# Kernel tuning notes

Hardware: AMD Instinct MI355X
Metric: run time of the kernel (lower is better)

## Reference

```python
import jax, jax.numpy as jnp
import numpy as np

B, E, D, L, R = 32, 30000, 200, 50, 474
GAMMA, ALPHA, BETA = 9.0, 0.3, 0.7


def _gate(x_ent, x_lit, Wg, bg, W1, W2, gate_bias):
    # Gate module: x = [x_ent; x_lit]; out = (1-g)*x_ent + g*tanh(Linear(x))
    x = jnp.concatenate([x_ent, x_lit], axis=-1)
    g_emb = jnp.tanh(x @ Wg.T + bg)
    g = jax.nn.sigmoid(x_ent @ W1.T + x_lit @ W2.T + gate_bias)
    return (1.0 - g) * x_ent + g * g_emb


def setup_inputs() -> dict:
    key = jax.random.key(0)
    ks = jax.random.split(key, 11)
    rn = lambda k, shape: jax.random.normal(k, shape, jnp.float32) * 0.05
    return {
        'e1': jax.random.randint(ks[0], (B,), 0, E),
        'rel': jax.random.randint(ks[1], (B,), 0, R),
        'e2_multi': jax.random.randint(ks[2], (B, E), 0, 2).astype(jnp.int32),
        'emb_e': rn(ks[3], (E, D)),
        'emb_rel': rn(ks[4], (R, D)),
        'num_lit': jax.random.uniform(ks[5], (E, L), jnp.float32),
        'Wg': rn(ks[6], (D, D + L)),
        'bg': jnp.zeros((D,), jnp.float32),
        'W1': rn(ks[7], (D, D)),
        'W2': rn(ks[8], (D, L)),
        'gate_bias': jnp.zeros((D,), jnp.float32),
        'prob': jax.random.uniform(ks[9], (B, E), jnp.float32),
        'drop_mask': jax.random.randint(ks[10], (B, E), 0, 2).astype(jnp.float32),
    }


def reference(e1, rel, e2_multi, emb_e, emb_rel, num_lit, Wg, bg, W1, W2,
              gate_bias, prob, drop_mask):
    e2m = e2_multi.astype(emb_e.dtype)  # [B, E] multi-hot labels
    # literal-gated embeddings (inp_drop treated as eval/identity)
    e1_emb = _gate(emb_e[e1], num_lit[e1], Wg, bg, W1, W2, gate_bias)   # [B, D]
    e2_emb = _gate(emb_e, num_lit, Wg, bg, W1, W2, gate_bias)           # [E, D]
    rel_emb = emb_rel[rel]                                              # [B, D]

    # our_loss: weighted masked means over the full entity table
    e2p = e2m * prob                                                    # [B, E]
    pos_mean = (e2p @ e2_emb) / e2p.sum(-1, keepdims=True)              # [B, D]
    pos_mean = ALPHA * pos_mean + (1.0 - ALPHA) * e1_emb
    inv = 1.0 - e2m
    inv_drop = inv * drop_mask * 2.0  # F.dropout(p=0.5) = mask * 1/(1-p)
    neg_mean = (inv_drop @ e2_emb) / inv.sum(-1, keepdims=True)
    neg_mean = BETA * neg_mean + (1.0 - BETA) * e1_emb

    q = e1_emb + rel_emb                                                # [B, D]
    pos_s = jnp.abs(q - pos_mean).sum(-1, keepdims=True)                # [B, 1]
    neg_s = jnp.abs(q - neg_mean).sum(-1)                               # [B]
    # faithful to torch: [B] - [B,1] broadcasts to [B,B]
    loss = -jnp.mean(jax.nn.log_sigmoid(neg_s - pos_s))

    # broadcast L1 distance to ALL entities: [B, E, D] intermediate
    score = GAMMA - jnp.abs(q[:, None, :] - e2_emb[None, :, :]).sum(-1)  # [B, E]
    pred = jax.nn.sigmoid(score)
    return (pred, loss)
```

## Files before the change

### kernel.cpp

```cpp
#include <hip/hip_runtime.h>
#include <hip/hip_bf16.h>
#include <cstddef>

constexpr int B = 32, E = 30000, D = 200, L = 50;

using short8 = __attribute__((ext_vector_type(8))) short;
using f32x4  = __attribute__((ext_vector_type(4))) float;

__device__ __forceinline__ float sigmoidf_(float x){ return 1.f/(1.f+__expf(-x)); }
__device__ __forceinline__ float tanhf_(float x){
    float t = __expf(-2.f*fabsf(x));
    return copysignf((1.f-t)/(1.f+t), x);
}
__device__ __forceinline__ unsigned short f2bf(float x){
    unsigned u = __float_as_uint(x);
    u += 0x7fffu + ((u>>16)&1u);
    return (unsigned short)(u>>16);
}
__device__ __forceinline__ float bf2f(unsigned short h){
    return __uint_as_float(((unsigned)h)<<16);
}

constexpr int WELEMS = 26*8*64*8;

__global__ __launch_bounds__(256) void wprep_kernel(
    const float* __restrict__ Wg, const float* __restrict__ W1,
    const float* __restrict__ W2,
    unsigned short* __restrict__ whi, unsigned short* __restrict__ wlo)
{
    int idx = blockIdx.x*256 + threadIdx.x;
    if (idx >= WELEMS) return;
    int j = idx & 7, l = (idx>>3)&63, ks = (idx>>9)&7, nt = idx>>12;
    int n = nt*16 + (l&15);
    int k = ks*32 + ((l>>4)&3)*8 + j;
    float v = 0.f;
    if (n < 208) {
        int d = n;
        if (d < 200 && k < 250) v = Wg[d*250 + k];
    } else {
        int d = n - 208;
        if (d < 200) {
            if (k < 200)      v = W1[d*200 + k];
            else if (k < 250) v = W2[d*50 + (k-200)];
        }
    }
    unsigned short h = f2bf(v);
    whi[idx] = h;
    wlo[idx] = f2bf(v - bf2f(h));
}

__global__ __launch_bounds__(256) void sums_kernel(
    const int* __restrict__ e2m, const float* __restrict__ prob,
    float* __restrict__ psum8, float* __restrict__ isum8)
{
    const int tid = threadIdx.x;
    const int b = blockIdx.x >> 3, ch = blockIdx.x & 7;
    const int es = ch * 3750;
    const int*   mrow = e2m  + (size_t)b * E + es;
    const float* prow = prob + (size_t)b * E + es;
    float sp = 0.f, si = 0.f;
    for (int i = tid; i < 3750; i += 256) {
        float m = (float)mrow[i];
        sp = fmaf(m, prow[i], sp);
        si += (1.f - m);
    }
    #pragma unroll
    for (int off = 32; off >= 1; off >>= 1) {
        sp += __shfl_down(sp, off);
        si += __shfl_down(si, off);
    }
    __shared__ float rp[4], ri[4];
    if ((tid & 63) == 0) { rp[tid >> 6] = sp; ri[tid >> 6] = si; }
    __syncthreads();
    if (tid == 0) {
        psum8[b*8 + ch] = rp[0] + rp[1] + rp[2] + rp[3];
        isum8[b*8 + ch] = ri[0] + ri[1] + ri[2] + ri[3];
    }
}

__global__ __launch_bounds__(512) void gate_kernel(
    const float* __restrict__ emb_e, const float* __restrict__ num_lit,
    const unsigned short* __restrict__ whi, const unsigned short* __restrict__ wlo,
    const float* __restrict__ bg, const float* __restrict__ gbias,
    float* __restrict__ e2_emb)
{
    __shared__ __align__(16) char smem[28672];
    unsigned short* Ah = (unsigned short*)smem;
    unsigned short* Al = (unsigned short*)(smem + 8192);
    float* PW = (float*)smem;

    const int tid  = threadIdx.x;
    const int lane = tid & 63;
    const int wid  = tid >> 6;
    const int mt   = wid & 3;
    const int g    = wid >> 2;
    const int mb   = blockIdx.x >> 1;
    const int h    = blockIdx.x & 1;
    const int e0   = mb * 64;
    const int start = h * 6;
    const int ntb  = start + g * 13;

    f32x4 acc[7];
    #pragma unroll
    for (int i = 0; i < 7; ++i) acc[i] = (f32x4){0.f,0.f,0.f,0.f};

    const int srow = tid >> 3;
    const int skq  = tid & 7;
    const int se   = e0 + srow;
    const int aoff = (((srow >> 4)*2 + (skq >> 2))*64 + ((srow & 15) | ((skq & 3) << 4)))*8;

#define WOFF(p, ks) (((size_t)(((ntb + (p))*8 + c*2 + (ks))*64 + lane))*8)

    for (int c = 0; c < 4; ++c) {
        float v[8];
        const int k0 = c*64 + skq*8;
        if (se < E) {
            if (k0 + 7 < 200) {
                float4 f0 = *(const float4*)(emb_e + (size_t)se*200 + k0);
                float4 f1 = *(const float4*)(emb_e + (size_t)se*200 + k0 + 4);
                v[0]=f0.x; v[1]=f0.y; v[2]=f0.z; v[3]=f0.w;
                v[4]=f1.x; v[5]=f1.y; v[6]=f1.z; v[7]=f1.w;
            } else {
                #pragma unroll
                for (int z = 0; z < 8; ++z) {
                    int kz = k0 + z;
                    v[z] = (kz < 250) ? num_lit[(size_t)se*50 + (kz - 200)] : 0.f;
                }
            }
        } else {
            #pragma unroll
            for (int z = 0; z < 8; ++z) v[z] = 0.f;
        }
        if (c) __syncthreads();
        short8 hv, lv;
        #pragma unroll
        for (int z = 0; z < 8; ++z) {
            unsigned short hh = f2bf(v[z]);
            hv[z] = (short)hh;
            lv[z] = (short)f2bf(v[z] - bf2f(hh));
        }
        *(short8*)&Ah[aoff] = hv;
        *(short8*)&Al[aoff] = lv;
        __syncthreads();

        short8 pwh[2][2], pwl[2][2];
        pwh[0][0] = *(const short8*)(whi + WOFF(0,0));
        pwh[0][1] = *(const short8*)(whi + WOFF(0,1));
        pwl[0][0] = *(const short8*)(wlo + WOFF(0,0));
        pwl[0][1] = *(const short8*)(wlo + WOFF(0,1));

        short8 xh[2], xl[2];
        #pragma unroll
        for (int ks = 0; ks < 2; ++ks) {
            int fo = ((mt*2 + ks)*64 + lane)*8;
            xh[ks] = *(const short8*)&Ah[fo];
            xl[ks] = *(const short8*)&Al[fo];
        }

        #pragma unroll
        for (int p = 0; p < 7; ++p) {
            const int cur = p & 1, nxt = cur ^ 1;
            if (p < 6) {
                pwh[nxt][0] = *(const short8*)(whi + WOFF(p+1,0));
                pwh[nxt][1] = *(const short8*)(whi + WOFF(p+1,1));
                pwl[nxt][0] = *(const short8*)(wlo + WOFF(p+1,0));
                pwl[nxt][1] = *(const short8*)(wlo + WOFF(p+1,1));
            }
            #pragma unroll
            for (int ks = 0; ks < 2; ++ks) {
                acc[p] = __builtin_amdgcn_mfma_f32_16x16x32_bf16(xh[ks], pwh[cur][ks], acc[p], 0,0,0);
                acc[p] = __builtin_amdgcn_mfma_f32_16x16x32_bf16(xl[ks], pwh[cur][ks], acc[p], 0,0,0);
                acc[p] = __builtin_amdgcn_mfma_f32_16x16x32_bf16(xh[ks], pwl[cur][ks], acc[p], 0,0,0);
            }
        }
    }
#undef WOFF

    __syncthreads();
    if (g == 1) {
        #pragma unroll
        for (int p = 0; p < 7; ++p)
            *(f32x4*)&PW[((mt*7 + p)*64 + lane)*4] = acc[p];
    }
    __syncthreads();
    if (g == 0) {
        const int col = lane & 15, rg = lane >> 4;
        #pragma unroll
        for (int p = 0; p < 7; ++p) {
            int d = (start + p)*16 + col;
            if (d >= 200) continue;
            float bgd = bg[d], gbd = gbias[d];
            f32x4 p2 = *(const f32x4*)&PW[((mt*7 + p)*64 + lane)*4];
            #pragma unroll
            for (int r = 0; r < 4; ++r) {
                int e = e0 + mt*16 + rg*4 + r;
                if (e >= E) continue;
                float pre1 = acc[p][r] + bgd;
                float pre2 = p2[r] + gbd;
                float gt = sigmoidf_(pre2);
                float t  = tanhf_(pre1);
                float emb = emb_e[(size_t)e*200 + d];
                e2_emb[(size_t)e*200 + d] = (1.f - gt)*emb + gt*t;
            }
        }
    }
}

__global__ __launch_bounds__(256) void q_kernel(
    const int* __restrict__ e1, const int* __restrict__ rel,
    const float* __restrict__ emb_rel, const float* __restrict__ e2_emb,
    float* __restrict__ q)
{
    int tid = threadIdx.x;
    for (int idx = tid; idx < B * D; idx += 256) {
        int b = idx / D, d = idx % D;
        q[idx] = e2_emb[(size_t)e1[b] * D + d] + emb_rel[(size_t)rel[b] * D + d];
    }
}

constexpr int GVB = 235;

__global__ __launch_bounds__(256) void gemv_kernel(
    const int* __restrict__ e2m, const float* __restrict__ prob,
    const float* __restrict__ drop, const float* __restrict__ e2_emb,
    float* __restrict__ gpart)
{
    __shared__ unsigned short Bf[13312];
    __shared__ unsigned short Acp[2048], Acn[2048];
    const int tid = threadIdx.x, lane = tid & 63, w = tid >> 6;
    const int e0 = blockIdx.x * 128;

    f32x4 acc[2][2][4];
    #pragma unroll
    for (int a = 0; a < 2; ++a)
        #pragma unroll
        for (int m = 0; m < 2; ++m)
            #pragma unroll
            for (int s = 0; s < 4; ++s) acc[a][m][s] = (f32x4){0.f,0.f,0.f,0.f};

    for (int c = 0; c < 2; ++c) {
        const int ec = e0 + c*64;
        if (c) __syncthreads();

        {
            const int bb = tid >> 3, part = tid & 7;
            const int eb = ec + part*8;
            float cp[8], cn[8];
            size_t base = (size_t)bb * E + eb;
            if (eb + 7 < E) {
                int4   m0 = *(const int4*)(e2m + base),   m1 = *(const int4*)(e2m + base + 4);
                float4 p0 = *(const float4*)(prob + base), p1 = *(const float4*)(prob + base + 4);
                float4 d0 = *(const float4*)(drop + base), d1 = *(const float4*)(drop + base + 4);
                cp[0]=m0.x?p0.x:0.f; cn[0]=m0.x?0.f:2.f*d0.x;
                cp[1]=m0.y?p0.y:0.f; cn[1]=m0.y?0.f:2.f*d0.y;
                cp[2]=m0.z?p0.z:0.f; cn[2]=m0.z?0.f:2.f*d0.z;
                cp[3]=m0.w?p0.w:0.f; cn[3]=m0.w?0.f:2.f*d0.w;
                cp[4]=m1.x?p1.x:0.f; cn[4]=m1.x?0.f:2.f*d1.x;
                cp[5]=m1.y?p1.y:0.f; cn[5]=m1.y?0.f:2.f*d1.y;
                cp[6]=m1.z?p1.z:0.f; cn[6]=m1.z?0.f:2.f*d1.z;
                cp[7]=m1.w?p1.w:0.f; cn[7]=m1.w?0.f:2.f*d1.w;
            } else {
                #pragma unroll
                for (int j = 0; j < 8; ++j) {
                    int e = eb + j;
                    cp[j] = 0.f; cn[j] = 0.f;
                    if (e < E) {
                        int m = e2m[base + j];
                        cp[j] = m ? prob[base + j] : 0.f;
                        cn[j] = m ? 0.f : 2.f * drop[base + j];
                    }
                }
            }
            short8 scp, scn;
            #pragma unroll
            for (int j = 0; j < 8; ++j) { scp[j] = (short)f2bf(cp[j]); scn[j] = (short)f2bf(cn[j]); }
            int off = (((bb >> 4)*2 + (part >> 2))*64 + ((bb & 15) | ((part & 3) << 4)))*8;
            *(short8*)&Acp[off] = scp;
            *(short8*)&Acn[off] = scn;
        }

        for (int s = tid; s < 3328; s += 256) {
            int el = s / 52, d4 = (s - el*52)*4;
            int e = ec + el;
            float4 f = make_float4(0.f,0.f,0.f,0.f);
            if (e < E && d4 < 200) f = *(const float4*)(e2_emb + (size_t)e*200 + d4);
            int ks = el >> 5, lp = (el >> 3) & 3, j = el & 7;
            float fv[4] = {f.x, f.y, f.z, f.w};
            #pragma unroll
            for (int z = 0; z < 4; ++z) {
                int d = d4 + z;
                Bf[(((d >> 4)*2 + ks)*64 + ((d & 15) | (lp << 4)))*8 + j] = f2bf(fv[z]);
            }
        }
        __syncthreads();

        short8 cpA[2][2], cnA[2][2];
        #pragma unroll
        for (int mtb = 0; mtb < 2; ++mtb)
            #pragma unroll
            for (int ks = 0; ks < 2; ++ks) {
                int fo = ((mtb*2 + ks)*64 + lane)*8;
                cpA[mtb][ks] = *(const short8*)&Acp[fo];
                cnA[mtb][ks] = *(const short8*)&Acn[fo];
            }
        #pragma unroll
        for (int ks = 0; ks < 2; ++ks)
            #pragma unroll
            for (int slot = 0; slot < 4; ++slot) {
                int nt = w + slot*4;
                if (nt < 13) {
                    short8 bf = *(const short8*)&Bf[((nt*2 + ks)*64 + lane)*8];
                    acc[0][0][slot] = __builtin_amdgcn_mfma_f32_16x16x32_bf16(cpA[0][ks], bf, acc[0][0][slot], 0,0,0);
                    acc[0][1][slot] = __builtin_amdgcn_mfma_f32_16x16x32_bf16(cpA[1][ks], bf, acc[0][1][slot], 0,0,0);
                    acc[1][0][slot] = __builtin_amdgcn_mfma_f32_16x16x32_bf16(cnA[0][ks], bf, acc[1][0][slot], 0,0,0);
                    acc[1][1][slot] = __builtin_amdgcn_mfma_f32_16x16x32_bf16(cnA[1][ks], bf, acc[1][1][slot], 0,0,0);
                }
            }
    }

    const int col = lane & 15, rg = lane >> 4;
    #pragma unroll
    for (int mat = 0; mat < 2; ++mat)
        #pragma unroll
        for (int mtb = 0; mtb < 2; ++mtb)
            #pragma unroll
            for (int slot = 0; slot < 4; ++slot) {
                int nt = w + slot*4;
                if (nt >= 13) continue;
                int d = nt*16 + col;
                if (d >= 200) continue;
                #pragma unroll
                for (int r = 0; r < 4; ++r) {
                    int b = mtb*16 + rg*4 + r;
                    gpart[(((size_t)blockIdx.x*2 + mat)*32 + b)*200 + d]
                        = acc[mat][mtb][slot][r];
                }
            }
}

__global__ __launch_bounds__(128) void gred_kernel(
    const float* __restrict__ gpart, float* __restrict__ posv, float* __restrict__ negv)
{
    int o = blockIdx.x*128 + threadIdx.x;
    float sp = 0.f, sn = 0.f;
    #pragma unroll 4
    for (int blk = 0; blk < GVB; ++blk) {
        sp += gpart[((size_t)blk*2 + 0)*6400 + o];
        sn += gpart[((size_t)blk*2 + 1)*6400 + o];
    }
    posv[o] = sp;
    negv[o] = sn;
}

__global__ __launch_bounds__(256) void score_kernel(
    const float* __restrict__ q, const float* __restrict__ e2_emb,
    float* __restrict__ pred)
{
    __shared__ __align__(16) float Qs[32*204];
    const int tid = threadIdx.x;
    const int e0 = blockIdx.x * 64;
    for (int i = tid; i < B*D; i += 256) {
        int b = i / 200, d = i - b*200;
        Qs[b*204 + d] = q[i];
    }
    __syncthreads();

    const int bgrp = tid & 7, egrp = tid >> 3;
    const int b0 = bgrp*4;
    const int ea = e0 + egrp*2, eb = ea + 1;
    const float* r0 = e2_emb + (size_t)(ea < E ? ea : E-1)*200;
    const float* r1 = e2_emb + (size_t)(eb < E ? eb : E-1)*200;

    float acc0[4] = {0.f,0.f,0.f,0.f}, acc1[4] = {0.f,0.f,0.f,0.f};
    #pragma unroll 5
    for (int dc = 0; dc < 200; dc += 8) {
        float4 a0 = *(const float4*)(r0 + dc);
        float4 a1 = *(const float4*)(r0 + dc + 4);
        float4 b0v = *(const float4*)(r1 + dc);
        float4 b1v = *(const float4*)(r1 + dc + 4);
        #pragma unroll
        for (int i = 0; i < 4; ++i) {
            float4 qa = *(const float4*)&Qs[(b0+i)*204 + dc];
            float4 qb = *(const float4*)&Qs[(b0+i)*204 + dc + 4];
            acc0[i] += fabsf(qa.x-a0.x) + fabsf(qa.y-a0.y) + fabsf(qa.z-a0.z) + fabsf(qa.w-a0.w)
                     + fabsf(qb.x-a1.x) + fabsf(qb.y-a1.y) + fabsf(qb.z-a1.z) + fabsf(qb.w-a1.w);
            acc1[i] += fabsf(qa.x-b0v.x) + fabsf(qa.y-b0v.y) + fabsf(qa.z-b0v.z) + fabsf(qa.w-b0v.w)
                     + fabsf(qb.x-b1v.x) + fabsf(qb.y-b1v.y) + fabsf(qb.z-b1v.z) + fabsf(qb.w-b1v.w);
        }
    }
    #pragma unroll
    for (int i = 0; i < 4; ++i) {
        if (ea < E) pred[(size_t)(b0+i)*E + ea] = sigmoidf_(9.0f - acc0[i]);
        if (eb < E) pred[(size_t)(b0+i)*E + eb] = sigmoidf_(9.0f - acc1[i]);
    }
}

__global__ __launch_bounds__(256) void final_kernel(
    const int* __restrict__ e1, const float* __restrict__ q,
    const float* __restrict__ posv, const float* __restrict__ negv,
    const float* __restrict__ psum8, const float* __restrict__ isum8,
    const float* __restrict__ e2_emb, float* __restrict__ loss_out)
{
    const int tid = threadIdx.x;
    __shared__ float SP[32], SI[32];
    if (tid < 32) {
        float s = 0.f, t = 0.f;
        #pragma unroll
        for (int k = 0; k < 8; ++k) { s += psum8[tid*8 + k]; t += isum8[tid*8 + k]; }
        SP[tid] = s; SI[tid] = t;
    }
    __syncthreads();

    const int b = tid >> 3, dl = tid & 7;
    const int e1b = e1[b];
    const float isp = 1.f / SP[b];
    const float isn = 1.f / SI[b];
    float ps = 0.f, ns = 0.f;
    #pragma unroll
    for (int t = 0; t < 25; ++t) {
        int d = dl*25 + t;
        float e1e = e2_emb[(size_t)e1b*200 + d];
        float pm = 0.3f * (posv[b*200 + d] * isp) + 0.7f * e1e;
        float nm = 0.7f * (negv[b*200 + d] * isn) + 0.3f * e1e;
        float qv = q[b*200 + d];
        ps += fabsf(qv - pm);
        ns += fabsf(qv - nm);
    }
    ps += __shfl_down(ps, 4, 8); ps += __shfl_down(ps, 2, 8); ps += __shfl_down(ps, 1, 8);
    ns += __shfl_down(ns, 4, 8); ns += __shfl_down(ns, 2, 8); ns += __shfl_down(ns, 1, 8);

    __shared__ float PS[B], NS[B];
    if (dl == 0) { PS[b] = ps; NS[b] = ns; }
    __syncthreads();

    float part = 0.f;
    #pragma unroll
    for (int r = 0; r < 4; ++r) {
        int idx = tid + r*256;
        int i = idx >> 5, j = idx & 31;
        float x = NS[j] - PS[i];
        part += fminf(x, 0.f) - log1pf(expf(-fabsf(x)));
    }
    #pragma unroll
    for (int off = 32; off >= 1; off >>= 1) part += __shfl_down(part, off);
    __shared__ float wr[4];
    if ((tid & 63) == 0) wr[tid >> 6] = part;
    __syncthreads();
    if (tid == 0) loss_out[0] = -(wr[0] + wr[1] + wr[2] + wr[3]) * (1.f/1024.f);
}

extern "C" void kernel_launch(void* const* d_in, const int* in_sizes, int n_in,
                              void* d_out, int out_size, void* d_ws, size_t ws_size,
                              hipStream_t stream)
{
    const int*   e1      = (const int*)d_in[0];
    const int*   rel     = (const int*)d_in[1];
    const int*   e2m     = (const int*)d_in[2];
    const float* emb_e   = (const float*)d_in[3];
    const float* emb_rel = (const float*)d_in[4];
    const float* num_lit = (const float*)d_in[5];
    const float* Wg      = (const float*)d_in[6];
    const float* bg      = (const float*)d_in[7];
    const float* W1      = (const float*)d_in[8];
    const float* W2      = (const float*)d_in[9];
    const float* gbias   = (const float*)d_in[10];
    const float* prob    = (const float*)d_in[11];
    const float* drop    = (const float*)d_in[12];

    float* pred = (float*)d_out;
    float* ws   = (float*)d_ws;

    float*          e2_emb = ws;
    float*          q      = ws + 6000000;
    unsigned short* whi    = (unsigned short*)(ws + 6006400);
    unsigned short* wlo    = (unsigned short*)(ws + 6059648);
    float*          gpart  = ws + 6112896;
    float*          posv   = ws + 9120896;
    float*          negv   = ws + 9127296;
    float*          psum8  = ws + 9133696;
    float*          isum8  = ws + 9133952;

    wprep_kernel<<<WELEMS/256, 256, 0, stream>>>(Wg, W1, W2, whi, wlo);
    sums_kernel<<<256, 256, 0, stream>>>(e2m, prob, psum8, isum8);
    gate_kernel<<<944, 512, 0, stream>>>(emb_e, num_lit, whi, wlo, bg, gbias, e2_emb);
    q_kernel<<<1, 256, 0, stream>>>(e1, rel, emb_rel, e2_emb, q);
    gemv_kernel<<<GVB, 256, 0, stream>>>(e2m, prob, drop, e2_emb, gpart);
    gred_kernel<<<50, 128, 0, stream>>>(gpart, posv, negv);
    score_kernel<<<(E + 63)/64, 256, 0, stream>>>(q, e2_emb, pred);
    final_kernel<<<1, 256, 0, stream>>>(e1, q, posv, negv, psum8, isum8, e2_emb,
                                        pred + (size_t)B*E);
}
```

Measured before the change: 268.3 us.

## Load gate A-fragments directly to registers and restage score kernel over entities

The gate kernel now loads each lane's MFMA A-fragment straight from global memory and splits it into bf16 hi/lo with a truncation-based perm split, dropping the LDS staging and per-chunk barriers. The score kernel switches to 512 threads, stages 64 entity rows in LDS, and reads q directly from global (uniform per wave, so it can broadcast), so each lane handles one entity and writes to pred are coalesced. The hi part now uses truncation instead of round-to-nearest, which can slightly change the precision of the hi/lo split. The score kernel's larger LDS footprint may reduce occupancy.

```diff
diff --git a/kernel.cpp b/kernel.cpp
--- a/kernel.cpp
+++ b/kernel.cpp
@@ -6,6 +6,7 @@
 
 using short8 = __attribute__((ext_vector_type(8))) short;
 using f32x4  = __attribute__((ext_vector_type(4))) float;
+using uint4v = __attribute__((ext_vector_type(4))) unsigned int;
 
 __device__ __forceinline__ float sigmoidf_(float x){ return 1.f/(1.f+__expf(-x)); }
 __device__ __forceinline__ float tanhf_(float x){
@@ -19,6 +20,20 @@
 }
 __device__ __forceinline__ float bf2f(unsigned short h){
     return __uint_as_float(((unsigned)h)<<16);
+}
+
+__device__ __forceinline__ void split8(const float* v, short8& hv, short8& lv) {
+    uint4v hp, lp;
+    #pragma unroll
+    for (int z = 0; z < 4; ++z) {
+        unsigned u0 = __float_as_uint(v[2*z]), u1 = __float_as_uint(v[2*z+1]);
+        hp[z] = __builtin_amdgcn_perm(u1, u0, 0x07060302u);
+        float r0 = v[2*z]   - __uint_as_float(u0 & 0xFFFF0000u);
+        float r1 = v[2*z+1] - __uint_as_float(u1 & 0xFFFF0000u);
+        lp[z] = __builtin_amdgcn_perm(__float_as_uint(r1), __float_as_uint(r0), 0x07060302u);
+    }
+    hv = __builtin_bit_cast(short8, hp);
+    lv = __builtin_bit_cast(short8, lp);
 }
 
 constexpr int WELEMS = 26*8*64*8;
@@ -84,10 +99,7 @@
     const float* __restrict__ bg, const float* __restrict__ gbias,
     float* __restrict__ e2_emb)
 {
-    __shared__ __align__(16) char smem[28672];
-    unsigned short* Ah = (unsigned short*)smem;
-    unsigned short* Al = (unsigned short*)(smem + 8192);
-    float* PW = (float*)smem;
+    __shared__ __align__(16) float PW[4*7*64*4];
 
     const int tid  = threadIdx.x;
     const int lane = tid & 63;
@@ -100,62 +112,53 @@
     const int start = h * 6;
     const int ntb  = start + g * 13;
 
+    const int arow = e0 + mt*16 + (lane & 15);
+    const int kgrp = ((lane >> 4) & 3) * 8;
+    const bool rok = arow < E;
+    const float* aeb = emb_e   + (size_t)arow * 200;
+    const float* alb = num_lit + (size_t)arow * 50;
+
     f32x4 acc[7];
     #pragma unroll
     for (int i = 0; i < 7; ++i) acc[i] = (f32x4){0.f,0.f,0.f,0.f};
 
-    const int srow = tid >> 3;
-    const int skq  = tid & 7;
-    const int se   = e0 + srow;
-    const int aoff = (((srow >> 4)*2 + (skq >> 2))*64 + ((srow & 15) | ((skq & 3) << 4)))*8;
-
 #define WOFF(p, ks) (((size_t)(((ntb + (p))*8 + c*2 + (ks))*64 + lane))*8)
 
     for (int c = 0; c < 4; ++c) {
-        float v[8];
-        const int k0 = c*64 + skq*8;
-        if (se < E) {
-            if (k0 + 7 < 200) {
-                float4 f0 = *(const float4*)(emb_e + (size_t)se*200 + k0);
-                float4 f1 = *(const float4*)(emb_e + (size_t)se*200 + k0 + 4);
+        short8 xh[2], xl[2];
+        #pragma unroll
+        for (int ks = 0; ks < 2; ++ks) {
+            const int k0 = c*64 + ks*32 + kgrp;
+            float v[8];
+            if (rok && k0 <= 192) {
+                float4 f0 = *(const float4*)(aeb + k0);
+                float4 f1 = *(const float4*)(aeb + k0 + 4);
                 v[0]=f0.x; v[1]=f0.y; v[2]=f0.z; v[3]=f0.w;
                 v[4]=f1.x; v[5]=f1.y; v[6]=f1.z; v[7]=f1.w;
+            } else if (rok && k0 <= 240) {
+                const int kl = k0 - 200;
+                #pragma unroll
+                for (int z = 0; z < 4; ++z) {
+                    float2 f = *(const float2*)(alb + kl + 2*z);
+                    v[2*z] = f.x; v[2*z+1] = f.y;
+                }
+            } else if (rok && k0 == 248) {
+                float2 f = *(const float2*)(alb + 48);
+                v[0] = f.x; v[1] = f.y;
+                #pragma unroll
+                for (int z = 2; z < 8; ++z) v[z] = 0.f;
             } else {
                 #pragma unroll
-                for (int z = 0; z < 8; ++z) {
-                    int kz = k0 + z;
-                    v[z] = (kz < 250) ? num_lit[(size_t)se*50 + (kz - 200)] : 0.f;
-                }
-            }
-        } else {
-            #pragma unroll
-            for (int z = 0; z < 8; ++z) v[z] = 0.f;
-        }
-        if (c) __syncthreads();
-        short8 hv, lv;
-        #pragma unroll
-        for (int z = 0; z < 8; ++z) {
-            unsigned short hh = f2bf(v[z]);
-            hv[z] = (short)hh;
-            lv[z] = (short)f2bf(v[z] - bf2f(hh));
-        }
-        *(short8*)&Ah[aoff] = hv;
-        *(short8*)&Al[aoff] = lv;
-        __syncthreads();
+                for (int z = 0; z < 8; ++z) v[z] = 0.f;
+            }
+            split8(v, xh[ks], xl[ks]);
+        }
 
         short8 pwh[2][2], pwl[2][2];
         pwh[0][0] = *(const short8*)(whi + WOFF(0,0));
         pwh[0][1] = *(const short8*)(whi + WOFF(0,1));
         pwl[0][0] = *(const short8*)(wlo + WOFF(0,0));
         pwl[0][1] = *(const short8*)(wlo + WOFF(0,1));
-
-        short8 xh[2], xl[2];
-        #pragma unroll
-        for (int ks = 0; ks < 2; ++ks) {
-            int fo = ((mt*2 + ks)*64 + lane)*8;
-            xh[ks] = *(const short8*)&Ah[fo];
-            xl[ks] = *(const short8*)&Al[fo];
-        }
 
         #pragma unroll
         for (int p = 0; p < 7; ++p) {
@@ -176,7 +179,6 @@
     }
 #undef WOFF
 
-    __syncthreads();
     if (g == 1) {
         #pragma unroll
         for (int p = 0; p < 7; ++p)
@@ -352,46 +354,43 @@
     negv[o] = sn;
 }
 
-__global__ __launch_bounds__(256) void score_kernel(
+__global__ __launch_bounds__(512) void score_kernel(
     const float* __restrict__ q, const float* __restrict__ e2_emb,
     float* __restrict__ pred)
 {
-    __shared__ __align__(16) float Qs[32*204];
-    const int tid = threadIdx.x;
+    __shared__ __align__(16) float Es[64*204];
+    const int tid = threadIdx.x, lane = tid & 63, w = tid >> 6;
     const int e0 = blockIdx.x * 64;
-    for (int i = tid; i < B*D; i += 256) {
-        int b = i / 200, d = i - b*200;
-        Qs[b*204 + d] = q[i];
-    }
-    __syncthreads();
-
-    const int bgrp = tid & 7, egrp = tid >> 3;
-    const int b0 = bgrp*4;
-    const int ea = e0 + egrp*2, eb = ea + 1;
-    const float* r0 = e2_emb + (size_t)(ea < E ? ea : E-1)*200;
-    const float* r1 = e2_emb + (size_t)(eb < E ? eb : E-1)*200;
-
-    float acc0[4] = {0.f,0.f,0.f,0.f}, acc1[4] = {0.f,0.f,0.f,0.f};
+
+    for (int s = tid; s < 64*50; s += 512) {
+        int er = s / 50, d4 = (s - er*50)*4;
+        int e = e0 + er;
+        float4 f = make_float4(0.f,0.f,0.f,0.f);
+        if (e < E) f = *(const float4*)(e2_emb + (size_t)e*200 + d4);
+        *(float4*)&Es[er*204 + d4] = f;
+    }
+    __syncthreads();
+
+    const int b0 = w * 4;
+    const float* erow = &Es[lane*204];
+    float acc[4] = {0.f,0.f,0.f,0.f};
     #pragma unroll 5
     for (int dc = 0; dc < 200; dc += 8) {
-        float4 a0 = *(const float4*)(r0 + dc);
-        float4 a1 = *(const float4*)(r0 + dc + 4);
-        float4 b0v = *(const float4*)(r1 + dc);
-        float4 b1v = *(const float4*)(r1 + dc + 4);
+        float4 ea = *(const float4*)(erow + dc);
+        float4 eb = *(const float4*)(erow + dc + 4);
         #pragma unroll
         for (int i = 0; i < 4; ++i) {
-            float4 qa = *(const float4*)&Qs[(b0+i)*204 + dc];
-            float4 qb = *(const float4*)&Qs[(b0+i)*204 + dc + 4];
-            acc0[i] += fabsf(qa.x-a0.x) + fabsf(qa.y-a0.y) + fabsf(qa.z-a0.z) + fabsf(qa.w-a0.w)
-                     + fabsf(qb.x-a1.x) + fabsf(qb.y-a1.y) + fabsf(qb.z-a1.z) + fabsf(qb.w-a1.w);
-            acc1[i] += fabsf(qa.x-b0v.x) + fabsf(qa.y-b0v.y) + fabsf(qa.z-b0v.z) + fabsf(qa.w-b0v.w)
-                     + fabsf(qb.x-b1v.x) + fabsf(qb.y-b1v.y) + fabsf(qb.z-b1v.z) + fabsf(qb.w-b1v.w);
-        }
-    }
-    #pragma unroll
-    for (int i = 0; i < 4; ++i) {
-        if (ea < E) pred[(size_t)(b0+i)*E + ea] = sigmoidf_(9.0f - acc0[i]);
-        if (eb < E) pred[(size_t)(b0+i)*E + eb] = sigmoidf_(9.0f - acc1[i]);
+            float4 qa = *(const float4*)(q + (b0+i)*200 + dc);
+            float4 qb = *(const float4*)(q + (b0+i)*200 + dc + 4);
+            acc[i] += fabsf(qa.x-ea.x) + fabsf(qa.y-ea.y) + fabsf(qa.z-ea.z) + fabsf(qa.w-ea.w)
+                    + fabsf(qb.x-eb.x) + fabsf(qb.y-eb.y) + fabsf(qb.z-eb.z) + fabsf(qb.w-eb.w);
+        }
+    }
+    int e = e0 + lane;
+    if (e < E) {
+        #pragma unroll
+        for (int i = 0; i < 4; ++i)
+            pred[(size_t)(b0+i)*E + e] = sigmoidf_(9.0f - acc[i]);
     }
 }
 
@@ -486,7 +485,7 @@
     q_kernel<<<1, 256, 0, stream>>>(e1, rel, emb_rel, e2_emb, q);
     gemv_kernel<<<GVB, 256, 0, stream>>>(e2m, prob, drop, e2_emb, gpart);
     gred_kernel<<<50, 128, 0, stream>>>(gpart, posv, negv);
-    score_kernel<<<(E + 63)/64, 256, 0, stream>>>(q, e2_emb, pred);
+    score_kernel<<<(E + 63)/64, 512, 0, stream>>>(q, e2_emb, pred);
     final_kernel<<<1, 256, 0, stream>>>(e1, q, posv, negv, psum8, isum8, e2_emb,
                                         pred + (size_t)B*E);
 }
```

Measured after the change: 272.4 us. Within noise of the previous version (+1.5%).
